# Kernel tuning notes

Hardware: AMD Instinct MI355X
Metric: run time of the kernel (lower is better)

Reference implementation:

```python
import jax, jax.numpy as jnp
import numpy as np

EPS = 1e-8  # torch F.cosine_similarity clamps norms to eps=1e-8

def _normalize(x):
    n = jnp.linalg.norm(x, axis=-1, keepdims=True)
    return x / jnp.maximum(n, EPS)

def _masked_mean(v, mask):
    m = mask.astype(v.dtype)
    return jnp.sum(v * m, axis=-1) / jnp.sum(m, axis=-1)

def setup_inputs() -> dict:
    key = jax.random.key(0)
    k1, k2 = jax.random.split(key)
    B, L1, L2, D = 128, 512, 512, 512
    x1 = jax.random.normal(k1, (B, L1, D), dtype=jnp.float32)
    x2 = jax.random.normal(k2, (B, L2, D), dtype=jnp.float32)
    mask1 = jnp.ones((B, L1), dtype=jnp.int32)
    mask2 = jnp.ones((B, L2), dtype=jnp.int32)
    return {"x1": x1, "mask1": mask1, "x2": x2, "mask2": mask2}

def reference(x1, mask1, x2, mask2):
    # normalized token embeddings
    n1 = _normalize(x1)  # (B, L1, D)
    n2 = _normalize(x2)  # (B, L2, D)
    # masked pairwise cosine similarity (B, L1, L2)
    sim = jnp.einsum('bld,bmd->blm', n1, n2)
    neg_inf = jnp.array(-jnp.inf, dtype=sim.dtype)
    sim = jnp.where(mask1[:, :, None].astype(bool), sim, neg_inf)
    sim = jnp.where(mask2[:, None, :].astype(bool), sim, neg_inf)
    # dual argmax (indices are constants w.r.t. grads, matching torch.no_grad)
    idx1 = jnp.argmax(sim, axis=-1)  # (B, L1): best x2 token per x1 token
    idx2 = jnp.argmax(sim, axis=-2)  # (B, L2): best x1 token per x2 token
    # gather matched partners and recompute per-token cosine sim
    g2 = jnp.take_along_axis(n2, idx1[:, :, None], axis=1)  # (B, L1, D)
    g1 = jnp.take_along_axis(n1, idx2[:, :, None], axis=1)  # (B, L2, D)
    sim1 = jnp.sum(n1 * g2, axis=-1)  # (B, L1)
    sim2 = jnp.sum(g1 * n2, axis=-1)  # (B, L2)
    s1 = _masked_mean(sim1, mask1)
    s2 = _masked_mean(sim2, mask2)
    return (s1 + s2) / 2  # (B,)
```

## Files before the change

kernel.cpp:

```cpp
#include <hip/hip_runtime.h>
#include <hip/hip_bf16.h>

#define NB 128
#define LL 512
#define DD 512

typedef __attribute__((ext_vector_type(4))) float  f32x4;
typedef __attribute__((ext_vector_type(8))) short  s16x8;

__device__ __forceinline__ short f2bf(float f) {
    __hip_bfloat16 h = __float2bfloat16(f);
    return *reinterpret_cast<short*>(&h);
}

__device__ __forceinline__ unsigned fmap(float f) {
    unsigned u = __float_as_uint(f);
    return (u & 0x80000000u) ? ~u : (u | 0x80000000u);
}
__device__ __forceinline__ float funmap(unsigned u) {
    unsigned b = (u & 0x80000000u) ? (u ^ 0x80000000u) : ~u;
    return __uint_as_float(b);
}

__global__ __launch_bounds__(256) void init_kernel(unsigned* __restrict__ p, int n) {
    int i = blockIdx.x * 256 + threadIdx.x;
    if (i < n) p[i] = 0u;
}

__global__ __launch_bounds__(256, 4) void simgemm_fused(
        const float* __restrict__ x1, const float* __restrict__ x2,
        const int* __restrict__ mask1, const int* __restrict__ mask2,
        unsigned* __restrict__ rowmax_u, unsigned* __restrict__ colmax_u) {
    __shared__ __align__(16) char lds[33792];
    char* As0 = lds;
    char* Bs0 = lds + 16384;
    float* invA_lds = reinterpret_cast<float*>(lds + 32768);
    float* invB_lds = reinterpret_cast<float*>(lds + 33280);

    int bid = blockIdx.x;
    int lid = (bid & 7) * 256 + (bid >> 3);
    int b   = lid >> 4;
    int tr  = (lid >> 2) & 3;
    int tc  = lid & 3;

    int tid  = threadIdx.x;
    int lane = tid & 63;
    int w    = tid >> 6;
    int wr = w >> 1, wc = w & 1;
    int l15 = lane & 15, lhi = lane >> 4;
    int rg3 = lane >> 3, sl = lane & 7;

    const float* Ab = x1 + ((size_t)b * LL + tr * 128) * DD;
    const float* Bb = x2 + ((size_t)b * LL + tc * 128) * DD;

    float ssa[4] = {0.f, 0.f, 0.f, 0.f};
    float ssb[4] = {0.f, 0.f, 0.f, 0.f};

    f32x4 acc[4][4];
    #pragma unroll
    for (int fr = 0; fr < 4; ++fr)
        #pragma unroll
        for (int fc = 0; fc < 4; ++fc) {
            acc[fr][fc].x = 0.f; acc[fr][fc].y = 0.f;
            acc[fr][fc].z = 0.f; acc[fr][fc].w = 0.f;
        }

    #define STAGE(src, dst, ss, t)                                                \
        {                                                                         \
            f32x4 v[4][2];                                                        \
            _Pragma("unroll")                                                     \
            for (int i = 0; i < 4; ++i) {                                         \
                int row = w * 32 + i * 8 + rg3;                                   \
                const float* g = (src) + (size_t)row * DD + (t) * 64 + sl * 8;    \
                v[i][0] = *reinterpret_cast<const f32x4*>(g);                     \
                v[i][1] = *reinterpret_cast<const f32x4*>(g + 4);                 \
            }                                                                     \
            _Pragma("unroll")                                                     \
            for (int i = 0; i < 4; ++i) {                                         \
                int row = w * 32 + i * 8 + rg3;                                   \
                f32x4 v0 = v[i][0], v1 = v[i][1];                                 \
                ss[i] += v0.x*v0.x + v0.y*v0.y + v0.z*v0.z + v0.w*v0.w            \
                       + v1.x*v1.x + v1.y*v1.y + v1.z*v1.z + v1.w*v1.w;           \
                s16x8 o;                                                          \
                o[0] = f2bf(v0.x); o[1] = f2bf(v0.y);                             \
                o[2] = f2bf(v0.z); o[3] = f2bf(v0.w);                             \
                o[4] = f2bf(v1.x); o[5] = f2bf(v1.y);                             \
                o[6] = f2bf(v1.z); o[7] = f2bf(v1.w);                             \
                unsigned byte = (unsigned)(row * 128 + sl * 16)                   \
                              ^ ((unsigned)(row & 7) << 4);                       \
                *reinterpret_cast<s16x8*>((dst) + byte) = o;                      \
            }                                                                     \
        }

    STAGE(Ab, As0, ssa, 0);
    STAGE(Bb, Bs0, ssb, 0);
    __syncthreads();

    for (int t = 0; t < 8; ++t) {
        #pragma unroll
        for (int ks = 0; ks < 2; ++ks) {
            s16x8 af[4], bf[4];
            #pragma unroll
            for (int fr = 0; fr < 4; ++fr) {
                int row = wr * 64 + fr * 16 + l15;
                unsigned byte = (unsigned)(row * 128 + ks * 64 + lhi * 16)
                              ^ ((unsigned)(row & 7) << 4);
                af[fr] = *reinterpret_cast<const s16x8*>(As0 + byte);
            }
            #pragma unroll
            for (int fc = 0; fc < 4; ++fc) {
                int crow = wc * 64 + fc * 16 + l15;
                unsigned byte = (unsigned)(crow * 128 + ks * 64 + lhi * 16)
                              ^ ((unsigned)(crow & 7) << 4);
                bf[fc] = *reinterpret_cast<const s16x8*>(Bs0 + byte);
            }
            __builtin_amdgcn_s_setprio(1);
            #pragma unroll
            for (int fr = 0; fr < 4; ++fr)
                #pragma unroll
                for (int fc = 0; fc < 4; ++fc)
                    acc[fr][fc] = __builtin_amdgcn_mfma_f32_16x16x32_bf16(
                        af[fr], bf[fc], acc[fr][fc], 0, 0, 0);
            __builtin_amdgcn_s_setprio(0);
        }
        __syncthreads();
        if (t < 7) {
            STAGE(Ab, As0, ssa, t + 1);
            STAGE(Bb, Bs0, ssb, t + 1);
            __syncthreads();
        }
    }

    #pragma unroll
    for (int i = 0; i < 4; ++i) {
        ssa[i] += __shfl_xor(ssa[i], 1, 64);
        ssa[i] += __shfl_xor(ssa[i], 2, 64);
        ssa[i] += __shfl_xor(ssa[i], 4, 64);
        ssb[i] += __shfl_xor(ssb[i], 1, 64);
        ssb[i] += __shfl_xor(ssb[i], 2, 64);
        ssb[i] += __shfl_xor(ssb[i], 4, 64);
    }
    if (sl == 0) {
        #pragma unroll
        for (int i = 0; i < 4; ++i) {
            int row = w * 32 + i * 8 + rg3;
            invA_lds[row] = 1.0f / fmaxf(sqrtf(ssa[i]), 1e-8f);
            invB_lds[row] = 1.0f / fmaxf(sqrtf(ssb[i]), 1e-8f);
        }
    }
    __syncthreads();

    float ia[4][4], ib4[4];
    #pragma unroll
    for (int fr = 0; fr < 4; ++fr)
        #pragma unroll
        for (int r = 0; r < 4; ++r)
            ia[fr][r] = invA_lds[wr * 64 + fr * 16 + lhi * 4 + r];
    #pragma unroll
    for (int fc = 0; fc < 4; ++fc)
        ib4[fc] = invB_lds[wc * 64 + fc * 16 + l15];
    #pragma unroll
    for (int fr = 0; fr < 4; ++fr)
        #pragma unroll
        for (int fc = 0; fc < 4; ++fc)
            #pragma unroll
            for (int r = 0; r < 4; ++r)
                acc[fr][fc][r] *= ia[fr][r] * ib4[fc];

    int m2[4];
    #pragma unroll
    for (int fc = 0; fc < 4; ++fc)
        m2[fc] = mask2[b * LL + tc * 128 + wc * 64 + fc * 16 + l15];
    int m1[4][4];
    #pragma unroll
    for (int fr = 0; fr < 4; ++fr)
        #pragma unroll
        for (int r = 0; r < 4; ++r)
            m1[fr][r] = mask1[b * LL + tr * 128 + wr * 64 + fr * 16 + lhi * 4 + r];

    #pragma unroll
    for (int fr = 0; fr < 4; ++fr) {
        #pragma unroll
        for (int r = 0; r < 4; ++r) {
            float v = -INFINITY;
            #pragma unroll
            for (int fc = 0; fc < 4; ++fc)
                if (m2[fc]) v = fmaxf(v, acc[fr][fc][r]);
            v = fmaxf(v, __shfl_xor(v, 1, 64));
            v = fmaxf(v, __shfl_xor(v, 2, 64));
            v = fmaxf(v, __shfl_xor(v, 4, 64));
            v = fmaxf(v, __shfl_xor(v, 8, 64));
            if (l15 == 0)
                atomicMax(&rowmax_u[b * LL + tr * 128 + wr * 64 + fr * 16 + lhi * 4 + r],
                          fmap(v));
        }
    }
    #pragma unroll
    for (int fc = 0; fc < 4; ++fc) {
        float v = -INFINITY;
        #pragma unroll
        for (int fr = 0; fr < 4; ++fr)
            #pragma unroll
            for (int r = 0; r < 4; ++r)
                if (m1[fr][r]) v = fmaxf(v, acc[fr][fc][r]);
        v = fmaxf(v, __shfl_xor(v, 16, 64));
        v = fmaxf(v, __shfl_xor(v, 32, 64));
        if (lhi == 0)
            atomicMax(&colmax_u[b * LL + tc * 128 + wc * 64 + fc * 16 + l15], fmap(v));
    }
    #undef STAGE
}

__global__ __launch_bounds__(64) void finalize_kernel(
        const unsigned* __restrict__ rowmax_u, const unsigned* __restrict__ colmax_u,
        const int* __restrict__ mask1, const int* __restrict__ mask2,
        float* __restrict__ out) {
    int b = blockIdx.x;
    int lane = threadIdx.x;
    float s1 = 0.f, c1 = 0.f, s2 = 0.f, c2 = 0.f;
    for (int i = lane; i < LL; i += 64) {
        if (mask1[b * LL + i]) { s1 += funmap(rowmax_u[b * LL + i]); c1 += 1.f; }
        if (mask2[b * LL + i]) { s2 += funmap(colmax_u[b * LL + i]); c2 += 1.f; }
    }
    #pragma unroll
    for (int off = 32; off >= 1; off >>= 1) {
        s1 += __shfl_xor(s1, off, 64);
        c1 += __shfl_xor(c1, off, 64);
        s2 += __shfl_xor(s2, off, 64);
        c2 += __shfl_xor(c2, off, 64);
    }
    if (lane == 0) out[b] = 0.5f * (s1 / c1 + s2 / c2);
}

extern "C" void kernel_launch(void* const* d_in, const int* in_sizes, int n_in,
                              void* d_out, int out_size, void* d_ws, size_t ws_size,
                              hipStream_t stream) {
    const float* x1    = (const float*)d_in[0];
    const int*   mask1 = (const int*)d_in[1];
    const float* x2    = (const float*)d_in[2];
    const int*   mask2 = (const int*)d_in[3];
    float* out = (float*)d_out;

    unsigned* rowmax_u = (unsigned*)d_ws;
    unsigned* colmax_u = rowmax_u + NB * LL;

    init_kernel<<<(2 * NB * LL + 255) / 256, 256, 0, stream>>>(rowmax_u, 2 * NB * LL);
    simgemm_fused<<<NB * 16, 256, 0, stream>>>(x1, x2, mask1, mask2,
                                               rowmax_u, colmax_u);
    finalize_kernel<<<NB, 64, 0, stream>>>(rowmax_u, colmax_u, mask1, mask2, out);
}
```

Measured before the change: 144.8 us.

## Prefetch next K-tile global loads into registers during MFMA compute

Global loads are now split from the LDS commit. The loads for tile t+1 are issued into registers before the MFMA loop on tile t, and the bf16 conversion and LDS store happen after the barrier. This is meant to hide global memory latency behind the matrix math of the current tile. It costs 64 extra VGPRs of prefetch buffers, so launch bounds drop from 4 to 3 blocks per SIMD group, which lowers occupancy.

```diff
diff --git a/kernel.cpp b/kernel.cpp
--- a/kernel.cpp
+++ b/kernel.cpp
@@ -27,7 +27,7 @@
     if (i < n) p[i] = 0u;
 }
 
-__global__ __launch_bounds__(256, 4) void simgemm_fused(
+__global__ __launch_bounds__(256, 3) void simgemm_fused(
         const float* __restrict__ x1, const float* __restrict__ x2,
         const int* __restrict__ mask1, const int* __restrict__ mask2,
         unsigned* __restrict__ rowmax_u, unsigned* __restrict__ colmax_u) {
@@ -56,6 +56,8 @@
     float ssa[4] = {0.f, 0.f, 0.f, 0.f};
     float ssb[4] = {0.f, 0.f, 0.f, 0.f};
 
+    f32x4 va[4][2], vb[4][2];
+
     f32x4 acc[4][4];
     #pragma unroll
     for (int fr = 0; fr < 4; ++fr)
@@ -65,38 +67,54 @@
             acc[fr][fc].z = 0.f; acc[fr][fc].w = 0.f;
         }
 
-    #define STAGE(src, dst, ss, t)                                                \
+    #define ISSUE(t)                                                              \
         {                                                                         \
-            f32x4 v[4][2];                                                        \
             _Pragma("unroll")                                                     \
             for (int i = 0; i < 4; ++i) {                                         \
                 int row = w * 32 + i * 8 + rg3;                                   \
-                const float* g = (src) + (size_t)row * DD + (t) * 64 + sl * 8;    \
-                v[i][0] = *reinterpret_cast<const f32x4*>(g);                     \
-                v[i][1] = *reinterpret_cast<const f32x4*>(g + 4);                 \
+                const float* ga = Ab + (size_t)row * DD + (t) * 64 + sl * 8;      \
+                va[i][0] = *reinterpret_cast<const f32x4*>(ga);                   \
+                va[i][1] = *reinterpret_cast<const f32x4*>(ga + 4);               \
+                const float* gb = Bb + (size_t)row * DD + (t) * 64 + sl * 8;      \
+                vb[i][0] = *reinterpret_cast<const f32x4*>(gb);                   \
+                vb[i][1] = *reinterpret_cast<const f32x4*>(gb + 4);               \
             }                                                                     \
+        }
+
+    #define COMMIT()                                                              \
+        {                                                                         \
             _Pragma("unroll")                                                     \
             for (int i = 0; i < 4; ++i) {                                         \
                 int row = w * 32 + i * 8 + rg3;                                   \
-                f32x4 v0 = v[i][0], v1 = v[i][1];                                 \
-                ss[i] += v0.x*v0.x + v0.y*v0.y + v0.z*v0.z + v0.w*v0.w            \
-                       + v1.x*v1.x + v1.y*v1.y + v1.z*v1.z + v1.w*v1.w;           \
-                s16x8 o;                                                          \
-                o[0] = f2bf(v0.x); o[1] = f2bf(v0.y);                             \
-                o[2] = f2bf(v0.z); o[3] = f2bf(v0.w);                             \
-                o[4] = f2bf(v1.x); o[5] = f2bf(v1.y);                             \
-                o[6] = f2bf(v1.z); o[7] = f2bf(v1.w);                             \
                 unsigned byte = (unsigned)(row * 128 + sl * 16)                   \
                               ^ ((unsigned)(row & 7) << 4);                       \
-                *reinterpret_cast<s16x8*>((dst) + byte) = o;                      \
+                f32x4 v0 = va[i][0], v1 = va[i][1];                               \
+                ssa[i] += v0.x*v0.x + v0.y*v0.y + v0.z*v0.z + v0.w*v0.w           \
+                        + v1.x*v1.x + v1.y*v1.y + v1.z*v1.z + v1.w*v1.w;          \
+                s16x8 oa;                                                         \
+                oa[0] = f2bf(v0.x); oa[1] = f2bf(v0.y);                           \
+                oa[2] = f2bf(v0.z); oa[3] = f2bf(v0.w);                           \
+                oa[4] = f2bf(v1.x); oa[5] = f2bf(v1.y);                           \
+                oa[6] = f2bf(v1.z); oa[7] = f2bf(v1.w);                           \
+                *reinterpret_cast<s16x8*>(As0 + byte) = oa;                       \
+                f32x4 u0 = vb[i][0], u1 = vb[i][1];                               \
+                ssb[i] += u0.x*u0.x + u0.y*u0.y + u0.z*u0.z + u0.w*u0.w           \
+                        + u1.x*u1.x + u1.y*u1.y + u1.z*u1.z + u1.w*u1.w;          \
+                s16x8 ob;                                                         \
+                ob[0] = f2bf(u0.x); ob[1] = f2bf(u0.y);                           \
+                ob[2] = f2bf(u0.z); ob[3] = f2bf(u0.w);                           \
+                ob[4] = f2bf(u1.x); ob[5] = f2bf(u1.y);                           \
+                ob[6] = f2bf(u1.z); ob[7] = f2bf(u1.w);                           \
+                *reinterpret_cast<s16x8*>(Bs0 + byte) = ob;                       \
             }                                                                     \
         }
 
-    STAGE(Ab, As0, ssa, 0);
-    STAGE(Bb, Bs0, ssb, 0);
+    ISSUE(0);
+    COMMIT();
     __syncthreads();
 
     for (int t = 0; t < 8; ++t) {
+        if (t < 7) ISSUE(t + 1);
         #pragma unroll
         for (int ks = 0; ks < 2; ++ks) {
             s16x8 af[4], bf[4];
@@ -125,8 +143,7 @@
         }
         __syncthreads();
         if (t < 7) {
-            STAGE(Ab, As0, ssa, t + 1);
-            STAGE(Bb, Bs0, ssb, t + 1);
+            COMMIT();
             __syncthreads();
         }
     }
@@ -208,7 +225,8 @@
         if (lhi == 0)
             atomicMax(&colmax_u[b * LL + tc * 128 + wc * 64 + fc * 16 + l15], fmap(v));
     }
-    #undef STAGE
+    #undef ISSUE
+    #undef COMMIT
 }
 
 __global__ __launch_bounds__(64) void finalize_kernel(
```

Result: slower. 249.1 us (+72.0%).
